# Kernel optimization log

Measured on AMD Instinct MI355X. Metric: run time of the kernel, lower is better.

## Reference

```python
import jax, jax.numpy as jnp
import numpy as np


def _flip_roll(a):
    # torch.roll(torch.flip(a, [-3,-2,-1]), (1,1,1), [-3,-2,-1])
    return jnp.roll(jnp.flip(a, axis=(-3, -2, -1)), shift=(1, 1, 1), axis=(-3, -2, -1))


def dht_3d(x):
    dims = (2, 3, 4)
    r = jnp.fft.fftn(x, axes=dims).real - jnp.fft.fftn(jnp.flip(x, axis=-1), axes=dims).imag
    norm = jnp.sqrt(jnp.sum(r * r, axis=dims, keepdims=True))
    safe = jnp.where(norm == 0, 1.0, norm)
    return jnp.where(norm != 0, r / safe, jnp.zeros_like(r))


def compl_mul3d(x1, x2):
    x1n = _flip_roll(x1)
    x2n = _flip_roll(x2)
    return 0.5 * (
        jnp.einsum('bixyz,ioxyz->boxyz', x1, x2)
        - jnp.einsum('bixyz,ioxyz->boxyz', x1n, x2n)
        + jnp.einsum('bixyz,ioxyz->boxyz', x1, x2n)
        + jnp.einsum('bixyz,ioxyz->boxyz', x1n, x2)
    )


def idht_3d(X):
    n = X.shape[2] * X.shape[3] * X.shape[4]
    return dht_3d(X) / n


def setup_inputs() -> dict:
    key = jax.random.key(0)
    k1, k2 = jax.random.split(key)
    B, Cin, Cout = 4, 32, 32
    S = 64
    M = 8
    scale = 1.0 / (Cin * Cout)
    x = jax.random.normal(k1, (B, Cin, S, S, S), dtype=jnp.float32)
    weights1 = scale * jax.random.uniform(k2, (Cin, Cout, M, M, M), dtype=jnp.float32)
    return {"x": x, "weights1": weights1}


def reference(x, weights1):
    B = x.shape[0]
    Cout = weights1.shape[1]
    m1, m2, m3 = weights1.shape[2], weights1.shape[3], weights1.shape[4]
    s1, s2, s3 = x.shape[-3], x.shape[-2], x.shape[-1]
    x_ht = dht_3d(x)
    conv = compl_mul3d(x_ht[:, :, :m1, :m2, :m3], weights1)
    out_ht = jnp.zeros((B, Cout, s1, s2, s3), dtype=x.dtype)
    out_ht = out_ht.at[:, :, :m1, :m2, :m3].set(conv)
    return idht_3d(out_ht)
```

## Files before the change

kernel.cpp:

```cpp
#include <hip/hip_runtime.h>
#include <math.h>


constexpr int NT = 262144;
constexpr float TWOPI_64 = 0.09817477042468103f;


__global__ __launch_bounds__(256) void k_fwd1(const float* __restrict__ x,
                                              float* __restrict__ S,
                                              float* __restrict__ red1p) {
  __shared__ float As[64 * 68];
  __shared__ float Bs[64 * 68];
  __shared__ float PL[32 * 65];
  __shared__ float tw1[1024];
  __shared__ float rsm[12];
  const int t = threadIdx.x;
  const int j = blockIdx.x;
  const int bc = blockIdx.y;
  const int n1a = j, n1b = (64 - j) & 63;
  const bool paired = (n1a != n1b);
  for (int u = t; u < 1024; u += 256) {
    int n3 = u >> 4, k3q = (u >> 2) & 3, jj = u & 3;
    int k3 = k3q + ((jj >> 1) << 2);
    float ang = TWOPI_64 * (float)((k3 * n3) & 63);
    tw1[u] = (jj & 1) ? sinf(ang) : cosf(ang);
  }
  const float4* xa4 = (const float4*)(x + ((size_t)bc << 18) + (n1a << 12));
  const float4* xb4 = (const float4*)(x + ((size_t)bc << 18) + (n1b << 12));
  float ssp = 0.f;
  for (int q = 0; q < 4; ++q) {
    int l4 = t + (q << 8);
    int fl = l4 << 2;
    int r = fl >> 6, c = fl & 63;
    float4 va = xa4[l4], vb = xb4[l4];
    *(float4*)&As[r * 68 + c] = va;
    *(float4*)&Bs[r * 68 + c] = vb;
    ssp += va.x * va.x + va.y * va.y + va.z * va.z + va.w * va.w;
    if (paired) ssp += vb.x * vb.x + vb.y * vb.y + vb.z * vb.z + vb.w * vb.w;
  }
  __syncthreads();
  const int n2 = t & 63;
  const int k3q = t >> 6;
  {
    float reA0 = 0, imA0 = 0, reA1 = 0, imA1 = 0;
    float reB0 = 0, imB0 = 0, reB1 = 0, imB1 = 0;
    const float4* Ar = (const float4*)&As[n2 * 68];
    const float4* Br = (const float4*)&Bs[n2 * 68];
    const float4* T4 = (const float4*)tw1;
    for (int m = 0; m < 16; ++m) {
      float4 va = Ar[m], vb = Br[m];
      float av[4] = {va.x, va.y, va.z, va.w};
      float bv[4] = {vb.x, vb.y, vb.z, vb.w};
#pragma unroll
      for (int e = 0; e < 4; ++e) {
        float4 tw = T4[(m << 4) + (e << 2) + k3q];
        float a = av[e], b = bv[e];
        reA0 += a * tw.x; imA0 -= a * tw.y;
        reB0 += b * tw.x; imB0 -= b * tw.y;
        reA1 += a * tw.z; imA1 -= a * tw.w;
        reB1 += b * tw.z; imB1 -= b * tw.w;
      }
    }
    PL[(k3q) * 65 + n2] = reA0;       PL[(8 + k3q) * 65 + n2] = imA0;
    PL[(16 + k3q) * 65 + n2] = reB0;  PL[(24 + k3q) * 65 + n2] = imB0;
    PL[(4 + k3q) * 65 + n2] = reA1;   PL[(12 + k3q) * 65 + n2] = imA1;
    PL[(20 + k3q) * 65 + n2] = reB1;  PL[(28 + k3q) * 65 + n2] = imB1;
  }
  float c1p = 0.f, c2p = 0.f;
  for (int q = 0; q < 16; ++q) {
    int l = t + (q << 8);
    int r = l >> 6, c = l & 63;
    float a = As[r * 68 + c];
    int m2 = (64 - r) & 63;
    int m3 = (64 - c) & 63;
    int m3b = (62 - c) & 63;
    c1p += a * Bs[m2 * 68 + m3];
    c2p += a * Bs[m2 * 68 + m3b];
  }
  if (paired) { c1p *= 2.f; c2p *= 2.f; }
  for (int off = 32; off; off >>= 1) {
    ssp += __shfl_down(ssp, off);
    c1p += __shfl_down(c1p, off);
    c2p += __shfl_down(c2p, off);
  }
  const int lane = t & 63, wid = t >> 6;
  if (lane == 0) { rsm[wid * 3] = ssp; rsm[wid * 3 + 1] = c1p; rsm[wid * 3 + 2] = c2p; }
  __syncthreads();
  if (t == 0) {
    red1p[((size_t)bc * 33 + j) * 3 + 0] = rsm[0] + rsm[3] + rsm[6] + rsm[9];
    red1p[((size_t)bc * 33 + j) * 3 + 1] = rsm[1] + rsm[4] + rsm[7] + rsm[10];
    red1p[((size_t)bc * 33 + j) * 3 + 2] = rsm[2] + rsm[5] + rsm[8] + rsm[11];
  }
  {
    const int k2 = t & 7;
    const int rr = t >> 3;
    const int row = rr >> 4, f = (rr >> 3) & 1, k3 = rr & 7;
    float re = 0.f, im = 0.f;
    const float* pr = &PL[rr * 65];
    const int tb = ((k2 & 3) << 2) + ((k2 >> 2) << 1);
#pragma unroll 4
    for (int n2i = 0; n2i < 64; ++n2i) {
      float v = pr[n2i];
      const float2 cs = *(const float2*)&tw1[(n2i << 4) + tb];
      re += v * cs.x; im -= v * cs.y;
    }
    const int n1row = row ? n1b : n1a;
    ((float2*)S)[(((size_t)bc * 64 + n1row) * 2 + f) * 64 + k2 * 8 + k3] =
        make_float2(re, im);
  }
}

__global__ __launch_bounds__(256) void k_fwd2s(const float* __restrict__ S,
                                               const float* __restrict__ red1p,
                                               float* __restrict__ xh) {
  __shared__ float2 U3L[256];
  __shared__ float2 tw[8 * 66];
  __shared__ float rbuf[99];
  const int t = threadIdx.x;
  const int h = blockIdx.x;
  const int bc = blockIdx.y;
  for (int u = t; u < 512; u += 256) {
    int k1 = u >> 6, n1 = u & 63;
    float ang = TWOPI_64 * (float)((k1 * n1) & 63);
    tw[k1 * 66 + n1] = make_float2(cosf(ang), sinf(ang));
  }
  if (t < 99) rbuf[t] = red1p[(size_t)bc * 99 + t];
  __syncthreads();
  {
    const int kkl = t & 15;
    const int f = (t >> 4) & 1;
    const int k1 = t >> 5;
    const int rr2 = f * 64 + h * 16 + kkl;
    const float2* Sb = (const float2*)(S + ((size_t)bc << 14));
    const float2* tk = &tw[k1 * 66];
    float re = 0.f, im = 0.f;
#pragma unroll 4
    for (int n1 = 0; n1 < 64; ++n1) {
      float2 ab = Sb[(n1 << 7) + rr2];
      float2 cs = tk[n1];
      re += ab.x * cs.x + ab.y * cs.y;
      im += ab.y * cs.x - ab.x * cs.y;
    }
    U3L[f * 128 + k1 * 16 + kkl] = make_float2(re, im);
  }
  __syncthreads();
  float ss = 0.f, c1 = 0.f, c2 = 0.f;
  for (int jj = 0; jj < 33; ++jj) {
    ss += rbuf[jj * 3];
    c1 += rbuf[jj * 3 + 1];
    c2 += rbuf[jj * 3 + 2];
  }
  float nsq = 0.5f * (float)NT * (2.f * ss + c1 - c2);
  float inv1 = nsq > 0.f ? rsqrtf(nsq) : 0.f;
  if (t < 128) {
    const int k1 = t >> 4, kkl = t & 15;
    const int kk = h * 16 + kkl;
    const int k3 = kk & 7;
    float2 U = U3L[k1 * 16 + kkl];
    float2 V = U3L[128 + k1 * 16 + kkl];
    float2 cs = tw[k3 * 66 + 1];
    float r = U.x - V.y - cs.y * (U.x + V.y) - cs.x * (U.y - V.x);
    xh[(size_t)bc * 512 + k1 * 64 + kk] = r * inv1;
  }
}

__global__ __launch_bounds__(256) void k_mixA(const float* __restrict__ xh,
                                              const float* __restrict__ w,
                                              float* __restrict__ A1,
                                              float* __restrict__ inv2q) {
  __shared__ float xsh[16384];
  __shared__ float convL[8 * 33];
  __shared__ float c64v[64], s64v[64];
  __shared__ float psum[4];
  const int t = threadIdx.x;
  const int bh = blockIdx.x;
  const int h = bh & 1;
  const int bc2 = bh >> 1;
  const int b = bc2 >> 5, o = bc2 & 31;
  if (t < 64) { float ang = TWOPI_64 * t; c64v[t] = cosf(ang); s64v[t] = sinf(ang); }
  const float4* xb4 = (const float4*)(xh + ((size_t)b << 14));
  float4* xs4 = (float4*)xsh;
  for (int q = 0; q < 16; ++q) xs4[t + (q << 8)] = xb4[t + (q << 8)];
  __syncthreads();
  const int n1m = t >> 5;
  const int col32 = t & 31;
  const int col = (h << 5) + col32;
  const int n2 = col >> 3, n3 = col & 7;
  const int k = (n1m << 6) + col;
  const int nk = (((8 - n1m) & 7) << 6) + (((8 - n2) & 7) << 3) + ((8 - n3) & 7);
  float acc = 0.f;
  const float* wb = w + ((size_t)o << 9);
#pragma unroll 4
  for (int i = 0; i < 32; ++i) {
    const float* wr = wb + ((size_t)i << 14);
    float xa = xsh[(i << 9) + k], xn = xsh[(i << 9) + nk];
    acc += (xa + xn) * wr[k] + (xa - xn) * wr[nk];
  }
  const float cval = 0.5f * acc;
  convL[n1m * 33 + col32] = cval;
  float p = cval * cval;
  for (int off = 32; off; off >>= 1) p += __shfl_down(p, off);
  if ((t & 63) == 0) psum[t >> 6] = p;
  __syncthreads();
  if (t == 0) {
    float Q = 2.f * (psum[0] + psum[1] + psum[2] + psum[3]);
    if (h == 0) { float c000 = convL[0]; Q += c000 * c000; }
    inv2q[bc2 * 2 + h] = Q;
  }
  const int q8 = t >> 5;
  float cv[8];
#pragma unroll
  for (int n1i = 0; n1i < 8; ++n1i) cv[n1i] = convL[n1i * 33 + col32];
  float2* A1p = (float2*)(A1 + ((size_t)bc2 << 13));
  for (int it = 0; it < 8; ++it) {
    const int k1 = q8 + (it << 3);
    float re = 0.f, im = 0.f;
#pragma unroll
    for (int n1i = 0; n1i < 8; ++n1i) {
      int a = (k1 * n1i) & 63;
      re += cv[n1i] * c64v[a];
      im -= cv[n1i] * s64v[a];
    }
    A1p[(k1 << 6) + col] = make_float2(re, im);
  }
}

__global__ __launch_bounds__(256) void k_expBC(const float* __restrict__ A1,
                                               const float* __restrict__ inv2q,
                                               float* __restrict__ out) {
  __shared__ float arow[128];
  __shared__ float B2[64 * 20];
  __shared__ float c64v[64], s64v[64];
  const int t = threadIdx.x;
  const int k1 = blockIdx.x;
  const int bc2 = blockIdx.y;
  const float q0 = inv2q[bc2 * 2], q1 = inv2q[bc2 * 2 + 1];
  if (t < 64) { float ang = TWOPI_64 * t; c64v[t] = cosf(ang); s64v[t] = sinf(ang); }
  if (t < 128) arow[t] = A1[((size_t)bc2 << 13) + (k1 << 7) + t];
  __syncthreads();
  {
    const int k2 = t & 63;
    const int g = t >> 6;
    const int f = g & 1;
    const int n3h = (g >> 1) << 2;
    float acc[4] = {0, 0, 0, 0};
    for (int n2i = 0; n2i < 8; ++n2i) {
      int a_ = (k2 * n2i) & 63;
      float tc = c64v[a_], ts = s64v[a_];
      const float4* ar4 = (const float4*)&arow[((n2i << 3) + n3h) << 1];
      float4 p0 = ar4[0];
      float4 p1 = ar4[1];
      if (f == 0) {
        acc[0] += p0.x * tc + p0.y * ts;
        acc[1] += p0.z * tc + p0.w * ts;
        acc[2] += p1.x * tc + p1.y * ts;
        acc[3] += p1.z * tc + p1.w * ts;
      } else {
        acc[0] += p0.y * tc - p0.x * ts;
        acc[1] += p0.w * tc - p0.z * ts;
        acc[2] += p1.y * tc - p1.x * ts;
        acc[3] += p1.w * tc - p1.z * ts;
      }
    }
    *(float4*)&B2[k2 * 20 + (f << 3) + n3h] = make_float4(acc[0], acc[1], acc[2], acc[3]);
  }
  __syncthreads();
  {
    const int k3 = t & 63;
    const int wid = t >> 6;
    float C1r[8], C2r[8];
#pragma unroll
    for (int n3 = 0; n3 < 8; ++n3) {
      int a0 = (k3 * n3) & 63;
      int a1 = (k3 * (n3 + 1)) & 63;
      C1r[n3] = c64v[a0] - s64v[a1];
      C2r[n3] = s64v[a0] - c64v[a1];
    }
    float nsq = 0.5f * (float)NT * (q0 + q1);
    const float sc = nsq > 0.f ? 1.f / (sqrtf(nsq) * (float)NT) : 0.f;
    float* dst = out + ((size_t)bc2 << 18) + (k1 << 12);
    for (int it = 0; it < 16; ++it) {
      int k2 = (wid << 4) + it;
      const float4* br4 = (const float4*)&B2[k2 * 20];
      float4 r0 = br4[0], r1 = br4[1], r2 = br4[2], r3 = br4[3];
      float acc = r0.x * C1r[0] + r0.y * C1r[1] + r0.z * C1r[2] + r0.w * C1r[3]
                + r1.x * C1r[4] + r1.y * C1r[5] + r1.z * C1r[6] + r1.w * C1r[7]
                + r2.x * C2r[0] + r2.y * C2r[1] + r2.z * C2r[2] + r2.w * C2r[3]
                + r3.x * C2r[4] + r3.y * C2r[5] + r3.z * C2r[6] + r3.w * C2r[7];
      dst[(k2 << 6) + k3] = acc * sc;
    }
  }
}

extern "C" void kernel_launch(void* const* d_in, const int* in_sizes, int n_in,
                              void* d_out, int out_size, void* d_ws, size_t ws_size,
                              hipStream_t stream) {
  const float* x = (const float*)d_in[0];
  const float* w = (const float*)d_in[1];
  float* out = (float*)d_out;
  float* ws = (float*)d_ws;
  float* S     = ws;
  float* red1p = ws + 2097152;
  float* xh    = ws + 2109824;
  float* inv2q = ws + 2175360;
  float* A1    = ws + 2175616;

  k_fwd1 <<<dim3(33, 128), 256, 0, stream>>>(x, S, red1p);
  k_fwd2s<<<dim3(4, 128),  256, 0, stream>>>(S, red1p, xh);
  k_mixA <<<dim3(256),     256, 0, stream>>>(xh, w, A1, inv2q);
  k_expBC<<<dim3(64, 128), 256, 0, stream>>>(A1, inv2q, out);
}
```

Baseline: 271.3 us.

## Fuse four stage kernels into one persistent kernel with grid barriers

Replaces the four separate launches with a single persistent kernel of 528 blocks that loops over the former grid work and separates the stages with atomic-counter grid barriers. It also swaps the per-element twiddle table lookups in the second forward DFT for a complex-rotation recurrence, and changes the PL padding so it can be read as float4. The mix stage now reads xh straight from global memory instead of staging it in shared memory. This removes launch gaps and tail effects between stages, but it depends on all 528 blocks being co-resident, pays for spin-wait barriers, and the recurrence may build up rounding error.

```diff
diff --git a/kernel.cpp b/kernel.cpp
--- a/kernel.cpp
+++ b/kernel.cpp
@@ -4,290 +4,317 @@
 
 constexpr int NT = 262144;
 constexpr float TWOPI_64 = 0.09817477042468103f;
-
-
-__global__ __launch_bounds__(256) void k_fwd1(const float* __restrict__ x,
-                                              float* __restrict__ S,
-                                              float* __restrict__ red1p) {
-  __shared__ float As[64 * 68];
-  __shared__ float Bs[64 * 68];
-  __shared__ float PL[32 * 65];
-  __shared__ float tw1[1024];
-  __shared__ float rsm[12];
+constexpr int NBLK = 528;
+
+
+__global__ void k_zero(int* __restrict__ cnt) {
+  if (threadIdx.x < 8) cnt[threadIdx.x] = 0;
+}
+
+__device__ __forceinline__ void gridbar(int* cnt, int ph) {
+  __syncthreads();
+  if (threadIdx.x == 0) {
+    __threadfence();
+    atomicAdd(&cnt[ph], 1);
+    while (atomicAdd(&cnt[ph], 0) < NBLK) __builtin_amdgcn_s_sleep(4);
+    __threadfence();
+  }
+  __syncthreads();
+}
+
+__global__ __launch_bounds__(256, 3) void k_mega(
+    const float* __restrict__ x, const float* __restrict__ w,
+    float* __restrict__ out, float* __restrict__ S, float* __restrict__ red1p,
+    float* __restrict__ xh, float* __restrict__ inv2q, float* __restrict__ A1,
+    int* __restrict__ cnt) {
+  __shared__ float smem[11916];
   const int t = threadIdx.x;
-  const int j = blockIdx.x;
-  const int bc = blockIdx.y;
-  const int n1a = j, n1b = (64 - j) & 63;
-  const bool paired = (n1a != n1b);
-  for (int u = t; u < 1024; u += 256) {
-    int n3 = u >> 4, k3q = (u >> 2) & 3, jj = u & 3;
-    int k3 = k3q + ((jj >> 1) << 2);
-    float ang = TWOPI_64 * (float)((k3 * n3) & 63);
-    tw1[u] = (jj & 1) ? sinf(ang) : cosf(ang);
-  }
-  const float4* xa4 = (const float4*)(x + ((size_t)bc << 18) + (n1a << 12));
-  const float4* xb4 = (const float4*)(x + ((size_t)bc << 18) + (n1b << 12));
-  float ssp = 0.f;
-  for (int q = 0; q < 4; ++q) {
-    int l4 = t + (q << 8);
-    int fl = l4 << 2;
-    int r = fl >> 6, c = fl & 63;
-    float4 va = xa4[l4], vb = xb4[l4];
-    *(float4*)&As[r * 68 + c] = va;
-    *(float4*)&Bs[r * 68 + c] = vb;
-    ssp += va.x * va.x + va.y * va.y + va.z * va.z + va.w * va.w;
-    if (paired) ssp += vb.x * vb.x + vb.y * vb.y + vb.z * vb.z + vb.w * vb.w;
-  }
-  __syncthreads();
-  const int n2 = t & 63;
-  const int k3q = t >> 6;
+  const int blk = blockIdx.x;
+
   {
-    float reA0 = 0, imA0 = 0, reA1 = 0, imA1 = 0;
-    float reB0 = 0, imB0 = 0, reB1 = 0, imB1 = 0;
-    const float4* Ar = (const float4*)&As[n2 * 68];
-    const float4* Br = (const float4*)&Bs[n2 * 68];
-    const float4* T4 = (const float4*)tw1;
-    for (int m = 0; m < 16; ++m) {
-      float4 va = Ar[m], vb = Br[m];
-      float av[4] = {va.x, va.y, va.z, va.w};
-      float bv[4] = {vb.x, vb.y, vb.z, vb.w};
+    float* As  = smem;
+    float* Bs  = smem + 4352;
+    float* PL  = smem + 8704;
+    float* tw1 = smem + 10880;
+    float* rsm = smem + 11904;
+    for (int u = t; u < 1024; u += 256) {
+      int n3 = u >> 4, k3q = (u >> 2) & 3, jj = u & 3;
+      int k3 = k3q + ((jj >> 1) << 2);
+      float ang = TWOPI_64 * (float)((k3 * n3) & 63);
+      tw1[u] = (jj & 1) ? sinf(ang) : cosf(ang);
+    }
+    const int k2s = t & 7;
+    const float angs = TWOPI_64 * (float)k2s;
+    const float dc2 = cosf(angs), ds2 = sinf(angs);
+    const int n2 = t & 63;
+    const int k3q = t >> 6;
+
+    for (int vb = blk; vb < 4224; vb += NBLK) {
+      const int bc = vb / 33;
+      const int j = vb - bc * 33;
+      const int n1a = j, n1b = (64 - j) & 63;
+      const bool paired = (n1a != n1b);
+      const float4* xa4 = (const float4*)(x + ((size_t)bc << 18) + (n1a << 12));
+      const float4* xb4 = (const float4*)(x + ((size_t)bc << 18) + (n1b << 12));
+      float ssp = 0.f;
+      for (int q = 0; q < 4; ++q) {
+        int l4 = t + (q << 8);
+        int fl = l4 << 2;
+        int r = fl >> 6, c = fl & 63;
+        float4 va = xa4[l4], vb4 = xb4[l4];
+        *(float4*)&As[r * 68 + c] = va;
+        *(float4*)&Bs[r * 68 + c] = vb4;
+        ssp += va.x * va.x + va.y * va.y + va.z * va.z + va.w * va.w;
+        if (paired) ssp += vb4.x * vb4.x + vb4.y * vb4.y + vb4.z * vb4.z + vb4.w * vb4.w;
+      }
+      __syncthreads();
+      {
+        float reA0 = 0, imA0 = 0, reA1 = 0, imA1 = 0;
+        float reB0 = 0, imB0 = 0, reB1 = 0, imB1 = 0;
+        const float4* Ar = (const float4*)&As[n2 * 68];
+        const float4* Br = (const float4*)&Bs[n2 * 68];
+        const float4* T4 = (const float4*)tw1;
+        for (int m = 0; m < 16; ++m) {
+          float4 va = Ar[m], vb4 = Br[m];
+          float av[4] = {va.x, va.y, va.z, va.w};
+          float bv[4] = {vb4.x, vb4.y, vb4.z, vb4.w};
 #pragma unroll
-      for (int e = 0; e < 4; ++e) {
-        float4 tw = T4[(m << 4) + (e << 2) + k3q];
-        float a = av[e], b = bv[e];
-        reA0 += a * tw.x; imA0 -= a * tw.y;
-        reB0 += b * tw.x; imB0 -= b * tw.y;
-        reA1 += a * tw.z; imA1 -= a * tw.w;
-        reB1 += b * tw.z; imB1 -= b * tw.w;
-      }
-    }
-    PL[(k3q) * 65 + n2] = reA0;       PL[(8 + k3q) * 65 + n2] = imA0;
-    PL[(16 + k3q) * 65 + n2] = reB0;  PL[(24 + k3q) * 65 + n2] = imB0;
-    PL[(4 + k3q) * 65 + n2] = reA1;   PL[(12 + k3q) * 65 + n2] = imA1;
-    PL[(20 + k3q) * 65 + n2] = reB1;  PL[(28 + k3q) * 65 + n2] = imB1;
-  }
-  float c1p = 0.f, c2p = 0.f;
-  for (int q = 0; q < 16; ++q) {
-    int l = t + (q << 8);
-    int r = l >> 6, c = l & 63;
-    float a = As[r * 68 + c];
-    int m2 = (64 - r) & 63;
-    int m3 = (64 - c) & 63;
-    int m3b = (62 - c) & 63;
-    c1p += a * Bs[m2 * 68 + m3];
-    c2p += a * Bs[m2 * 68 + m3b];
-  }
-  if (paired) { c1p *= 2.f; c2p *= 2.f; }
-  for (int off = 32; off; off >>= 1) {
-    ssp += __shfl_down(ssp, off);
-    c1p += __shfl_down(c1p, off);
-    c2p += __shfl_down(c2p, off);
-  }
-  const int lane = t & 63, wid = t >> 6;
-  if (lane == 0) { rsm[wid * 3] = ssp; rsm[wid * 3 + 1] = c1p; rsm[wid * 3 + 2] = c2p; }
-  __syncthreads();
-  if (t == 0) {
-    red1p[((size_t)bc * 33 + j) * 3 + 0] = rsm[0] + rsm[3] + rsm[6] + rsm[9];
-    red1p[((size_t)bc * 33 + j) * 3 + 1] = rsm[1] + rsm[4] + rsm[7] + rsm[10];
-    red1p[((size_t)bc * 33 + j) * 3 + 2] = rsm[2] + rsm[5] + rsm[8] + rsm[11];
-  }
+          for (int e = 0; e < 4; ++e) {
+            float4 tw = T4[(m << 4) + (e << 2) + k3q];
+            float a = av[e], b = bv[e];
+            reA0 += a * tw.x; imA0 -= a * tw.y;
+            reB0 += b * tw.x; imB0 -= b * tw.y;
+            reA1 += a * tw.z; imA1 -= a * tw.w;
+            reB1 += b * tw.z; imB1 -= b * tw.w;
+          }
+        }
+        PL[(k3q) * 68 + n2] = reA0;       PL[(8 + k3q) * 68 + n2] = imA0;
+        PL[(16 + k3q) * 68 + n2] = reB0;  PL[(24 + k3q) * 68 + n2] = imB0;
+        PL[(4 + k3q) * 68 + n2] = reA1;   PL[(12 + k3q) * 68 + n2] = imA1;
+        PL[(20 + k3q) * 68 + n2] = reB1;  PL[(28 + k3q) * 68 + n2] = imB1;
+      }
+      float c1p = 0.f, c2p = 0.f;
+      for (int q = 0; q < 16; ++q) {
+        int l = t + (q << 8);
+        int r = l >> 6, c = l & 63;
+        float a = As[r * 68 + c];
+        int m2 = (64 - r) & 63;
+        int m3 = (64 - c) & 63;
+        int m3b = (62 - c) & 63;
+        c1p += a * Bs[m2 * 68 + m3];
+        c2p += a * Bs[m2 * 68 + m3b];
+      }
+      if (paired) { c1p *= 2.f; c2p *= 2.f; }
+      for (int off = 32; off; off >>= 1) {
+        ssp += __shfl_down(ssp, off);
+        c1p += __shfl_down(c1p, off);
+        c2p += __shfl_down(c2p, off);
+      }
+      const int lane = t & 63, wid = t >> 6;
+      if (lane == 0) { rsm[wid * 3] = ssp; rsm[wid * 3 + 1] = c1p; rsm[wid * 3 + 2] = c2p; }
+      __syncthreads();
+      if (t == 0) {
+        red1p[((size_t)bc * 33 + j) * 3 + 0] = rsm[0] + rsm[3] + rsm[6] + rsm[9];
+        red1p[((size_t)bc * 33 + j) * 3 + 1] = rsm[1] + rsm[4] + rsm[7] + rsm[10];
+        red1p[((size_t)bc * 33 + j) * 3 + 2] = rsm[2] + rsm[5] + rsm[8] + rsm[11];
+      }
+      {
+        const int rr = t >> 3;
+        const int row = rr >> 4, f = (rr >> 3) & 1, k3 = rr & 7;
+        float rc = 1.f, rs = 0.f, re = 0.f, im = 0.f;
+        const float4* pr4 = (const float4*)&PL[rr * 68];
+#pragma unroll 4
+        for (int m = 0; m < 16; ++m) {
+          float4 v = pr4[m];
+          re += v.x * rc; im -= v.x * rs;
+          { float nc = rc * dc2 - rs * ds2; rs = rs * dc2 + rc * ds2; rc = nc; }
+          re += v.y * rc; im -= v.y * rs;
+          { float nc = rc * dc2 - rs * ds2; rs = rs * dc2 + rc * ds2; rc = nc; }
+          re += v.z * rc; im -= v.z * rs;
+          { float nc = rc * dc2 - rs * ds2; rs = rs * dc2 + rc * ds2; rc = nc; }
+          re += v.w * rc; im -= v.w * rs;
+          { float nc = rc * dc2 - rs * ds2; rs = rs * dc2 + rc * ds2; rc = nc; }
+        }
+        const int n1row = row ? n1b : n1a;
+        ((float2*)S)[(((size_t)bc * 64 + n1row) * 2 + f) * 64 + k2s * 8 + k3] =
+            make_float2(re, im);
+      }
+    }
+  }
+  gridbar(cnt, 0);
+
+  if (blk < 512) {
+    const int h = blk & 3;
+    const int bc = blk >> 2;
+    float2* U3L = (float2*)smem;
+    float2* tw2 = (float2*)(smem + 512);
+    float* rbuf = smem + 1568;
+    for (int u = t; u < 512; u += 256) {
+      int k1 = u >> 6, n1 = u & 63;
+      float ang = TWOPI_64 * (float)((k1 * n1) & 63);
+      tw2[k1 * 66 + n1] = make_float2(cosf(ang), sinf(ang));
+    }
+    if (t < 99) rbuf[t] = red1p[(size_t)bc * 99 + t];
+    __syncthreads();
+    {
+      const int kkl = t & 15;
+      const int f = (t >> 4) & 1;
+      const int k1 = t >> 5;
+      const int rr2 = f * 64 + h * 16 + kkl;
+      const float2* Sb = (const float2*)(S + ((size_t)bc << 14));
+      const float2* tk = &tw2[k1 * 66];
+      float re = 0.f, im = 0.f;
+#pragma unroll 4
+      for (int n1 = 0; n1 < 64; ++n1) {
+        float2 ab = Sb[(n1 << 7) + rr2];
+        float2 cs = tk[n1];
+        re += ab.x * cs.x + ab.y * cs.y;
+        im += ab.y * cs.x - ab.x * cs.y;
+      }
+      U3L[f * 128 + k1 * 16 + kkl] = make_float2(re, im);
+    }
+    __syncthreads();
+    float ss = 0.f, c1 = 0.f, c2 = 0.f;
+    for (int jj = 0; jj < 33; ++jj) {
+      ss += rbuf[jj * 3];
+      c1 += rbuf[jj * 3 + 1];
+      c2 += rbuf[jj * 3 + 2];
+    }
+    float nsq = 0.5f * (float)NT * (2.f * ss + c1 - c2);
+    float inv1 = nsq > 0.f ? rsqrtf(nsq) : 0.f;
+    if (t < 128) {
+      const int k1w = t >> 4, kkl2 = t & 15;
+      const int kk = h * 16 + kkl2;
+      const int k3 = kk & 7;
+      float2 U = U3L[k1w * 16 + kkl2];
+      float2 V = U3L[128 + k1w * 16 + kkl2];
+      float2 cs = tw2[k3 * 66 + 1];
+      float r = U.x - V.y - cs.y * (U.x + V.y) - cs.x * (U.y - V.x);
+      xh[(size_t)bc * 512 + k1w * 64 + kk] = r * inv1;
+    }
+  }
+  gridbar(cnt, 1);
+
+  if (((blk & 1) == 0) && blk < 512) {
+    const int bh = blk >> 1;
+    const int h = bh & 1;
+    const int bc2 = bh >> 1;
+    const int b = bc2 >> 5, o = bc2 & 31;
+    float* convL = smem;
+    float* c64v = smem + 264;
+    float* s64v = smem + 328;
+    float* psum = smem + 392;
+    if (t < 64) { float ang = TWOPI_64 * t; c64v[t] = cosf(ang); s64v[t] = sinf(ang); }
+    const float* xg = xh + ((size_t)b << 14);
+    const int n1m = t >> 5;
+    const int col32 = t & 31;
+    const int col = (h << 5) + col32;
+    const int n2 = col >> 3, n3 = col & 7;
+    const int k = (n1m << 6) + col;
+    const int nk = (((8 - n1m) & 7) << 6) + (((8 - n2) & 7) << 3) + ((8 - n3) & 7);
+    float acc = 0.f;
+    const float* wb = w + ((size_t)o << 9);
+#pragma unroll 4
+    for (int i = 0; i < 32; ++i) {
+      const float* wr = wb + ((size_t)i << 14);
+      float xa = xg[(i << 9) + k], xn = xg[(i << 9) + nk];
+      acc += (xa + xn) * wr[k] + (xa - xn) * wr[nk];
+    }
+    const float cval = 0.5f * acc;
+    convL[n1m * 33 + col32] = cval;
+    float p = cval * cval;
+    for (int off = 32; off; off >>= 1) p += __shfl_down(p, off);
+    if ((t & 63) == 0) psum[t >> 6] = p;
+    __syncthreads();
+    if (t == 0) {
+      float Q = 2.f * (psum[0] + psum[1] + psum[2] + psum[3]);
+      if (h == 0) { float c000 = convL[0]; Q += c000 * c000; }
+      inv2q[bc2 * 2 + h] = Q;
+    }
+    const int q8 = t >> 5;
+    float cv[8];
+#pragma unroll
+    for (int n1i = 0; n1i < 8; ++n1i) cv[n1i] = convL[n1i * 33 + col32];
+    float2* A1p = (float2*)(A1 + ((size_t)bc2 << 13));
+    for (int it = 0; it < 8; ++it) {
+      const int k1 = q8 + (it << 3);
+      float re = 0.f, im = 0.f;
+#pragma unroll
+      for (int n1i = 0; n1i < 8; ++n1i) {
+        int a = (k1 * n1i) & 63;
+        re += cv[n1i] * c64v[a];
+        im -= cv[n1i] * s64v[a];
+      }
+      A1p[(k1 << 6) + col] = make_float2(re, im);
+    }
+  }
+  gridbar(cnt, 2);
+
   {
-    const int k2 = t & 7;
-    const int rr = t >> 3;
-    const int row = rr >> 4, f = (rr >> 3) & 1, k3 = rr & 7;
-    float re = 0.f, im = 0.f;
-    const float* pr = &PL[rr * 65];
-    const int tb = ((k2 & 3) << 2) + ((k2 >> 2) << 1);
-#pragma unroll 4
-    for (int n2i = 0; n2i < 64; ++n2i) {
-      float v = pr[n2i];
-      const float2 cs = *(const float2*)&tw1[(n2i << 4) + tb];
-      re += v * cs.x; im -= v * cs.y;
-    }
-    const int n1row = row ? n1b : n1a;
-    ((float2*)S)[(((size_t)bc * 64 + n1row) * 2 + f) * 64 + k2 * 8 + k3] =
-        make_float2(re, im);
-  }
-}
-
-__global__ __launch_bounds__(256) void k_fwd2s(const float* __restrict__ S,
-                                               const float* __restrict__ red1p,
-                                               float* __restrict__ xh) {
-  __shared__ float2 U3L[256];
-  __shared__ float2 tw[8 * 66];
-  __shared__ float rbuf[99];
-  const int t = threadIdx.x;
-  const int h = blockIdx.x;
-  const int bc = blockIdx.y;
-  for (int u = t; u < 512; u += 256) {
-    int k1 = u >> 6, n1 = u & 63;
-    float ang = TWOPI_64 * (float)((k1 * n1) & 63);
-    tw[k1 * 66 + n1] = make_float2(cosf(ang), sinf(ang));
-  }
-  if (t < 99) rbuf[t] = red1p[(size_t)bc * 99 + t];
-  __syncthreads();
-  {
-    const int kkl = t & 15;
-    const int f = (t >> 4) & 1;
-    const int k1 = t >> 5;
-    const int rr2 = f * 64 + h * 16 + kkl;
-    const float2* Sb = (const float2*)(S + ((size_t)bc << 14));
-    const float2* tk = &tw[k1 * 66];
-    float re = 0.f, im = 0.f;
-#pragma unroll 4
-    for (int n1 = 0; n1 < 64; ++n1) {
-      float2 ab = Sb[(n1 << 7) + rr2];
-      float2 cs = tk[n1];
-      re += ab.x * cs.x + ab.y * cs.y;
-      im += ab.y * cs.x - ab.x * cs.y;
-    }
-    U3L[f * 128 + k1 * 16 + kkl] = make_float2(re, im);
-  }
-  __syncthreads();
-  float ss = 0.f, c1 = 0.f, c2 = 0.f;
-  for (int jj = 0; jj < 33; ++jj) {
-    ss += rbuf[jj * 3];
-    c1 += rbuf[jj * 3 + 1];
-    c2 += rbuf[jj * 3 + 2];
-  }
-  float nsq = 0.5f * (float)NT * (2.f * ss + c1 - c2);
-  float inv1 = nsq > 0.f ? rsqrtf(nsq) : 0.f;
-  if (t < 128) {
-    const int k1 = t >> 4, kkl = t & 15;
-    const int kk = h * 16 + kkl;
-    const int k3 = kk & 7;
-    float2 U = U3L[k1 * 16 + kkl];
-    float2 V = U3L[128 + k1 * 16 + kkl];
-    float2 cs = tw[k3 * 66 + 1];
-    float r = U.x - V.y - cs.y * (U.x + V.y) - cs.x * (U.y - V.x);
-    xh[(size_t)bc * 512 + k1 * 64 + kk] = r * inv1;
-  }
-}
-
-__global__ __launch_bounds__(256) void k_mixA(const float* __restrict__ xh,
-                                              const float* __restrict__ w,
-                                              float* __restrict__ A1,
-                                              float* __restrict__ inv2q) {
-  __shared__ float xsh[16384];
-  __shared__ float convL[8 * 33];
-  __shared__ float c64v[64], s64v[64];
-  __shared__ float psum[4];
-  const int t = threadIdx.x;
-  const int bh = blockIdx.x;
-  const int h = bh & 1;
-  const int bc2 = bh >> 1;
-  const int b = bc2 >> 5, o = bc2 & 31;
-  if (t < 64) { float ang = TWOPI_64 * t; c64v[t] = cosf(ang); s64v[t] = sinf(ang); }
-  const float4* xb4 = (const float4*)(xh + ((size_t)b << 14));
-  float4* xs4 = (float4*)xsh;
-  for (int q = 0; q < 16; ++q) xs4[t + (q << 8)] = xb4[t + (q << 8)];
-  __syncthreads();
-  const int n1m = t >> 5;
-  const int col32 = t & 31;
-  const int col = (h << 5) + col32;
-  const int n2 = col >> 3, n3 = col & 7;
-  const int k = (n1m << 6) + col;
-  const int nk = (((8 - n1m) & 7) << 6) + (((8 - n2) & 7) << 3) + ((8 - n3) & 7);
-  float acc = 0.f;
-  const float* wb = w + ((size_t)o << 9);
-#pragma unroll 4
-  for (int i = 0; i < 32; ++i) {
-    const float* wr = wb + ((size_t)i << 14);
-    float xa = xsh[(i << 9) + k], xn = xsh[(i << 9) + nk];
-    acc += (xa + xn) * wr[k] + (xa - xn) * wr[nk];
-  }
-  const float cval = 0.5f * acc;
-  convL[n1m * 33 + col32] = cval;
-  float p = cval * cval;
-  for (int off = 32; off; off >>= 1) p += __shfl_down(p, off);
-  if ((t & 63) == 0) psum[t >> 6] = p;
-  __syncthreads();
-  if (t == 0) {
-    float Q = 2.f * (psum[0] + psum[1] + psum[2] + psum[3]);
-    if (h == 0) { float c000 = convL[0]; Q += c000 * c000; }
-    inv2q[bc2 * 2 + h] = Q;
-  }
-  const int q8 = t >> 5;
-  float cv[8];
-#pragma unroll
-  for (int n1i = 0; n1i < 8; ++n1i) cv[n1i] = convL[n1i * 33 + col32];
-  float2* A1p = (float2*)(A1 + ((size_t)bc2 << 13));
-  for (int it = 0; it < 8; ++it) {
-    const int k1 = q8 + (it << 3);
-    float re = 0.f, im = 0.f;
-#pragma unroll
-    for (int n1i = 0; n1i < 8; ++n1i) {
-      int a = (k1 * n1i) & 63;
-      re += cv[n1i] * c64v[a];
-      im -= cv[n1i] * s64v[a];
-    }
-    A1p[(k1 << 6) + col] = make_float2(re, im);
-  }
-}
-
-__global__ __launch_bounds__(256) void k_expBC(const float* __restrict__ A1,
-                                               const float* __restrict__ inv2q,
-                                               float* __restrict__ out) {
-  __shared__ float arow[128];
-  __shared__ float B2[64 * 20];
-  __shared__ float c64v[64], s64v[64];
-  const int t = threadIdx.x;
-  const int k1 = blockIdx.x;
-  const int bc2 = blockIdx.y;
-  const float q0 = inv2q[bc2 * 2], q1 = inv2q[bc2 * 2 + 1];
-  if (t < 64) { float ang = TWOPI_64 * t; c64v[t] = cosf(ang); s64v[t] = sinf(ang); }
-  if (t < 128) arow[t] = A1[((size_t)bc2 << 13) + (k1 << 7) + t];
-  __syncthreads();
-  {
-    const int k2 = t & 63;
-    const int g = t >> 6;
-    const int f = g & 1;
-    const int n3h = (g >> 1) << 2;
-    float acc[4] = {0, 0, 0, 0};
-    for (int n2i = 0; n2i < 8; ++n2i) {
-      int a_ = (k2 * n2i) & 63;
-      float tc = c64v[a_], ts = s64v[a_];
-      const float4* ar4 = (const float4*)&arow[((n2i << 3) + n3h) << 1];
-      float4 p0 = ar4[0];
-      float4 p1 = ar4[1];
-      if (f == 0) {
-        acc[0] += p0.x * tc + p0.y * ts;
-        acc[1] += p0.z * tc + p0.w * ts;
-        acc[2] += p1.x * tc + p1.y * ts;
-        acc[3] += p1.z * tc + p1.w * ts;
-      } else {
-        acc[0] += p0.y * tc - p0.x * ts;
-        acc[1] += p0.w * tc - p0.z * ts;
-        acc[2] += p1.y * tc - p1.x * ts;
-        acc[3] += p1.w * tc - p1.z * ts;
-      }
-    }
-    *(float4*)&B2[k2 * 20 + (f << 3) + n3h] = make_float4(acc[0], acc[1], acc[2], acc[3]);
-  }
-  __syncthreads();
-  {
-    const int k3 = t & 63;
-    const int wid = t >> 6;
+    float* arow = smem;
+    float* B2 = smem + 128;
+    float* c64v = smem + 1408;
+    float* s64v = smem + 1472;
+    if (t < 64) { float ang = TWOPI_64 * t; c64v[t] = cosf(ang); s64v[t] = sinf(ang); }
+    __syncthreads();
+    const int k3c = t & 63;
+    const int widc = t >> 6;
     float C1r[8], C2r[8];
 #pragma unroll
     for (int n3 = 0; n3 < 8; ++n3) {
-      int a0 = (k3 * n3) & 63;
-      int a1 = (k3 * (n3 + 1)) & 63;
+      int a0 = (k3c * n3) & 63;
+      int a1 = (k3c * (n3 + 1)) & 63;
       C1r[n3] = c64v[a0] - s64v[a1];
       C2r[n3] = s64v[a0] - c64v[a1];
     }
-    float nsq = 0.5f * (float)NT * (q0 + q1);
-    const float sc = nsq > 0.f ? 1.f / (sqrtf(nsq) * (float)NT) : 0.f;
-    float* dst = out + ((size_t)bc2 << 18) + (k1 << 12);
-    for (int it = 0; it < 16; ++it) {
-      int k2 = (wid << 4) + it;
-      const float4* br4 = (const float4*)&B2[k2 * 20];
-      float4 r0 = br4[0], r1 = br4[1], r2 = br4[2], r3 = br4[3];
-      float acc = r0.x * C1r[0] + r0.y * C1r[1] + r0.z * C1r[2] + r0.w * C1r[3]
-                + r1.x * C1r[4] + r1.y * C1r[5] + r1.z * C1r[6] + r1.w * C1r[7]
-                + r2.x * C2r[0] + r2.y * C2r[1] + r2.z * C2r[2] + r2.w * C2r[3]
-                + r3.x * C2r[4] + r3.y * C2r[5] + r3.z * C2r[6] + r3.w * C2r[7];
-      dst[(k2 << 6) + k3] = acc * sc;
+    for (int vb = blk; vb < 8192; vb += NBLK) {
+      const int k1 = vb & 63, bc2 = vb >> 6;
+      if (t < 128) arow[t] = A1[((size_t)bc2 << 13) + (k1 << 7) + t];
+      __syncthreads();
+      {
+        const int k2 = t & 63;
+        const int g = t >> 6;
+        const int f = g & 1;
+        const int n3h = (g >> 1) << 2;
+        float accv[4] = {0, 0, 0, 0};
+        for (int n2i = 0; n2i < 8; ++n2i) {
+          int a_ = (k2 * n2i) & 63;
+          float tc = c64v[a_], ts = s64v[a_];
+          const float4* ar4 = (const float4*)&arow[((n2i << 3) + n3h) << 1];
+          float4 p0 = ar4[0];
+          float4 p1 = ar4[1];
+          if (f == 0) {
+            accv[0] += p0.x * tc + p0.y * ts;
+            accv[1] += p0.z * tc + p0.w * ts;
+            accv[2] += p1.x * tc + p1.y * ts;
+            accv[3] += p1.z * tc + p1.w * ts;
+          } else {
+            accv[0] += p0.y * tc - p0.x * ts;
+            accv[1] += p0.w * tc - p0.z * ts;
+            accv[2] += p1.y * tc - p1.x * ts;
+            accv[3] += p1.w * tc - p1.z * ts;
+          }
+        }
+        *(float4*)&B2[k2 * 20 + (f << 3) + n3h] =
+            make_float4(accv[0], accv[1], accv[2], accv[3]);
+      }
+      __syncthreads();
+      {
+        float q0 = inv2q[bc2 * 2], q1 = inv2q[bc2 * 2 + 1];
+        float nsq = 0.5f * (float)NT * (q0 + q1);
+        const float sc = nsq > 0.f ? 1.f / (sqrtf(nsq) * (float)NT) : 0.f;
+        float* dst = out + ((size_t)bc2 << 18) + (k1 << 12);
+        for (int it = 0; it < 16; ++it) {
+          int k2 = (widc << 4) + it;
+          const float4* br4 = (const float4*)&B2[k2 * 20];
+          float4 r0 = br4[0], r1 = br4[1], r2 = br4[2], r3 = br4[3];
+          float acc = r0.x * C1r[0] + r0.y * C1r[1] + r0.z * C1r[2] + r0.w * C1r[3]
+                    + r1.x * C1r[4] + r1.y * C1r[5] + r1.z * C1r[6] + r1.w * C1r[7]
+                    + r2.x * C2r[0] + r2.y * C2r[1] + r2.z * C2r[2] + r2.w * C2r[3]
+                    + r3.x * C2r[4] + r3.y * C2r[5] + r3.z * C2r[6] + r3.w * C2r[7];
+          dst[(k2 << 6) + k3c] = acc * sc;
+        }
+      }
     }
   }
 }
@@ -304,9 +331,8 @@
   float* xh    = ws + 2109824;
   float* inv2q = ws + 2175360;
   float* A1    = ws + 2175616;
-
-  k_fwd1 <<<dim3(33, 128), 256, 0, stream>>>(x, S, red1p);
-  k_fwd2s<<<dim3(4, 128),  256, 0, stream>>>(S, red1p, xh);
-  k_mixA <<<dim3(256),     256, 0, stream>>>(xh, w, A1, inv2q);
-  k_expBC<<<dim3(64, 128), 256, 0, stream>>>(A1, inv2q, out);
+  int*   cnt   = (int*)(ws + 3224192);
+
+  k_zero<<<1, 64, 0, stream>>>(cnt);
+  k_mega<<<dim3(NBLK), dim3(256), 0, stream>>>(x, w, out, S, red1p, xh, inv2q, A1, cnt);
 }
```

After: 438.7 us. 1.62x slower.

## Fuse spectral mix with inverse transform; use twiddle recurrence in forward pass

Applied to the files above, without the earlier changes.

The channel-mixing kernel and the inverse-expansion kernel are merged into one kernel launched on a (2,128) grid. Each block recomputes the full 512-point mode mix for its (batch, out-channel), computes the normalisation locally, and writes 32 k1 planes of the output. This drops the A1/inv2q workspace round trip, one launch, and the earlier xh shared-memory staging. In k_fwd1 the final 64-point DFT now generates twiddles with a complex rotation recurrence over float4 loads instead of reading them from the shared-memory table, and the PL row pitch is padded to 68. In exchange, the large output write now comes from only 256 blocks of 4 waves each, which may underuse memory bandwidth. The recurrence also adds a small amount of rounding drift.

```diff
diff --git a/kernel.cpp b/kernel.cpp
--- a/kernel.cpp
+++ b/kernel.cpp
@@ -11,7 +11,7 @@
                                               float* __restrict__ red1p) {
   __shared__ float As[64 * 68];
   __shared__ float Bs[64 * 68];
-  __shared__ float PL[32 * 65];
+  __shared__ float PL[32 * 68];
   __shared__ float tw1[1024];
   __shared__ float rsm[12];
   const int t = threadIdx.x;
@@ -25,6 +25,9 @@
     float ang = TWOPI_64 * (float)((k3 * n3) & 63);
     tw1[u] = (jj & 1) ? sinf(ang) : cosf(ang);
   }
+  const int k2s = t & 7;
+  const float angs = TWOPI_64 * (float)k2s;
+  const float dc2 = cosf(angs), ds2 = sinf(angs);
   const float4* xa4 = (const float4*)(x + ((size_t)bc << 18) + (n1a << 12));
   const float4* xb4 = (const float4*)(x + ((size_t)bc << 18) + (n1b << 12));
   float ssp = 0.f;
@@ -61,10 +64,10 @@
         reB1 += b * tw.z; imB1 -= b * tw.w;
       }
     }
-    PL[(k3q) * 65 + n2] = reA0;       PL[(8 + k3q) * 65 + n2] = imA0;
-    PL[(16 + k3q) * 65 + n2] = reB0;  PL[(24 + k3q) * 65 + n2] = imB0;
-    PL[(4 + k3q) * 65 + n2] = reA1;   PL[(12 + k3q) * 65 + n2] = imA1;
-    PL[(20 + k3q) * 65 + n2] = reB1;  PL[(28 + k3q) * 65 + n2] = imB1;
+    PL[(k3q) * 68 + n2] = reA0;       PL[(8 + k3q) * 68 + n2] = imA0;
+    PL[(16 + k3q) * 68 + n2] = reB0;  PL[(24 + k3q) * 68 + n2] = imB0;
+    PL[(4 + k3q) * 68 + n2] = reA1;   PL[(12 + k3q) * 68 + n2] = imA1;
+    PL[(20 + k3q) * 68 + n2] = reB1;  PL[(28 + k3q) * 68 + n2] = imB1;
   }
   float c1p = 0.f, c2p = 0.f;
   for (int q = 0; q < 16; ++q) {
@@ -92,20 +95,24 @@
     red1p[((size_t)bc * 33 + j) * 3 + 2] = rsm[2] + rsm[5] + rsm[8] + rsm[11];
   }
   {
-    const int k2 = t & 7;
     const int rr = t >> 3;
     const int row = rr >> 4, f = (rr >> 3) & 1, k3 = rr & 7;
-    float re = 0.f, im = 0.f;
-    const float* pr = &PL[rr * 65];
-    const int tb = ((k2 & 3) << 2) + ((k2 >> 2) << 1);
+    float rc = 1.f, rs = 0.f, re = 0.f, im = 0.f;
+    const float4* pr4 = (const float4*)&PL[rr * 68];
 #pragma unroll 4
-    for (int n2i = 0; n2i < 64; ++n2i) {
-      float v = pr[n2i];
-      const float2 cs = *(const float2*)&tw1[(n2i << 4) + tb];
-      re += v * cs.x; im -= v * cs.y;
+    for (int m = 0; m < 16; ++m) {
+      float4 v = pr4[m];
+      re += v.x * rc; im -= v.x * rs;
+      { float nc = rc * dc2 - rs * ds2; rs = rs * dc2 + rc * ds2; rc = nc; }
+      re += v.y * rc; im -= v.y * rs;
+      { float nc = rc * dc2 - rs * ds2; rs = rs * dc2 + rc * ds2; rc = nc; }
+      re += v.z * rc; im -= v.z * rs;
+      { float nc = rc * dc2 - rs * ds2; rs = rs * dc2 + rc * ds2; rc = nc; }
+      re += v.w * rc; im -= v.w * rs;
+      { float nc = rc * dc2 - rs * ds2; rs = rs * dc2 + rc * ds2; rc = nc; }
     }
     const int n1row = row ? n1b : n1a;
-    ((float2*)S)[(((size_t)bc * 64 + n1row) * 2 + f) * 64 + k2 * 8 + k3] =
+    ((float2*)S)[(((size_t)bc * 64 + n1row) * 2 + f) * 64 + k2s * 8 + k3] =
         make_float2(re, im);
   }
 }
@@ -164,130 +171,121 @@
   }
 }
 
-__global__ __launch_bounds__(256) void k_mixA(const float* __restrict__ xh,
-                                              const float* __restrict__ w,
-                                              float* __restrict__ A1,
-                                              float* __restrict__ inv2q) {
-  __shared__ float xsh[16384];
-  __shared__ float convL[8 * 33];
+__global__ __launch_bounds__(256) void k_mixexp(const float* __restrict__ xh,
+                                                const float* __restrict__ w,
+                                                float* __restrict__ out) {
+  __shared__ float convL[8 * 66];
+  __shared__ float A1L[32 * 132];
+  __shared__ float B2w[4 * 64 * 20];
   __shared__ float c64v[64], s64v[64];
   __shared__ float psum[4];
   const int t = threadIdx.x;
-  const int bh = blockIdx.x;
-  const int h = bh & 1;
-  const int bc2 = bh >> 1;
+  const int h = blockIdx.x;
+  const int bc2 = blockIdx.y;
   const int b = bc2 >> 5, o = bc2 & 31;
   if (t < 64) { float ang = TWOPI_64 * t; c64v[t] = cosf(ang); s64v[t] = sinf(ang); }
-  const float4* xb4 = (const float4*)(xh + ((size_t)b << 14));
-  float4* xs4 = (float4*)xsh;
-  for (int q = 0; q < 16; ++q) xs4[t + (q << 8)] = xb4[t + (q << 8)];
-  __syncthreads();
-  const int n1m = t >> 5;
-  const int col32 = t & 31;
-  const int col = (h << 5) + col32;
-  const int n2 = col >> 3, n3 = col & 7;
-  const int k = (n1m << 6) + col;
-  const int nk = (((8 - n1m) & 7) << 6) + (((8 - n2) & 7) << 3) + ((8 - n3) & 7);
-  float acc = 0.f;
+  const float* xg = xh + ((size_t)b << 14);
+  const int col = t & 63;
+  const int n1m = t >> 6;
+  const int n2c = col >> 3, n3c = col & 7;
+  const int nkc = (((8 - n2c) & 7) << 3) + ((8 - n3c) & 7);
+  const int k0 = t;
+  const int nk0 = (((8 - n1m) & 7) << 6) + nkc;
+  const int k1p = t + 256;
+  const int nk1 = (((8 - (n1m + 4)) & 7) << 6) + nkc;
+  float acc0 = 0.f, acc1 = 0.f;
   const float* wb = w + ((size_t)o << 9);
 #pragma unroll 4
   for (int i = 0; i < 32; ++i) {
     const float* wr = wb + ((size_t)i << 14);
-    float xa = xsh[(i << 9) + k], xn = xsh[(i << 9) + nk];
-    acc += (xa + xn) * wr[k] + (xa - xn) * wr[nk];
-  }
-  const float cval = 0.5f * acc;
-  convL[n1m * 33 + col32] = cval;
-  float p = cval * cval;
+    const float* xi = xg + (i << 9);
+    float xa0 = xi[k0], xn0 = xi[nk0];
+    float xa1 = xi[k1p], xn1 = xi[nk1];
+    acc0 += (xa0 + xn0) * wr[k0] + (xa0 - xn0) * wr[nk0];
+    acc1 += (xa1 + xn1) * wr[k1p] + (xa1 - xn1) * wr[nk1];
+  }
+  const float c0 = 0.5f * acc0, c1v = 0.5f * acc1;
+  convL[n1m * 66 + col] = c0;
+  convL[(n1m + 4) * 66 + col] = c1v;
+  float p = c0 * c0 + c1v * c1v;
   for (int off = 32; off; off >>= 1) p += __shfl_down(p, off);
   if ((t & 63) == 0) psum[t >> 6] = p;
   __syncthreads();
-  if (t == 0) {
-    float Q = 2.f * (psum[0] + psum[1] + psum[2] + psum[3]);
-    if (h == 0) { float c000 = convL[0]; Q += c000 * c000; }
-    inv2q[bc2 * 2 + h] = Q;
-  }
-  const int q8 = t >> 5;
+  const float S2 = psum[0] + psum[1] + psum[2] + psum[3];
+  const float c000 = convL[0];
+  const float nsq = 0.5f * (float)NT * (2.f * S2 + c000 * c000);
+  const float sc = nsq > 0.f ? 1.f / (sqrtf(nsq) * (float)NT) : 0.f;
+  const int wid = t >> 6, l = t & 63;
   float cv[8];
 #pragma unroll
-  for (int n1i = 0; n1i < 8; ++n1i) cv[n1i] = convL[n1i * 33 + col32];
-  float2* A1p = (float2*)(A1 + ((size_t)bc2 << 13));
+  for (int n1 = 0; n1 < 8; ++n1) cv[n1] = convL[n1 * 66 + l];
+#pragma unroll
   for (int it = 0; it < 8; ++it) {
-    const int k1 = q8 + (it << 3);
+    const int k1l = wid * 8 + it;
+    const int k1g = (h << 5) + k1l;
     float re = 0.f, im = 0.f;
 #pragma unroll
-    for (int n1i = 0; n1i < 8; ++n1i) {
-      int a = (k1 * n1i) & 63;
-      re += cv[n1i] * c64v[a];
-      im -= cv[n1i] * s64v[a];
-    }
-    A1p[(k1 << 6) + col] = make_float2(re, im);
-  }
-}
-
-__global__ __launch_bounds__(256) void k_expBC(const float* __restrict__ A1,
-                                               const float* __restrict__ inv2q,
-                                               float* __restrict__ out) {
-  __shared__ float arow[128];
-  __shared__ float B2[64 * 20];
-  __shared__ float c64v[64], s64v[64];
-  const int t = threadIdx.x;
-  const int k1 = blockIdx.x;
-  const int bc2 = blockIdx.y;
-  const float q0 = inv2q[bc2 * 2], q1 = inv2q[bc2 * 2 + 1];
-  if (t < 64) { float ang = TWOPI_64 * t; c64v[t] = cosf(ang); s64v[t] = sinf(ang); }
-  if (t < 128) arow[t] = A1[((size_t)bc2 << 13) + (k1 << 7) + t];
-  __syncthreads();
-  {
-    const int k2 = t & 63;
-    const int g = t >> 6;
-    const int f = g & 1;
-    const int n3h = (g >> 1) << 2;
-    float acc[4] = {0, 0, 0, 0};
+    for (int n1 = 0; n1 < 8; ++n1) {
+      int a = (k1g * n1) & 63;
+      re += cv[n1] * c64v[a];
+      im -= cv[n1] * s64v[a];
+    }
+    A1L[k1l * 132 + 2 * l] = re;
+    A1L[k1l * 132 + 2 * l + 1] = im;
+  }
+  asm volatile("s_waitcnt lgkmcnt(0)" ::: "memory");
+  float csc[8], css[8];
+#pragma unroll
+  for (int n2i = 0; n2i < 8; ++n2i) {
+    int a = (l * n2i) & 63;
+    csc[n2i] = c64v[a]; css[n2i] = s64v[a];
+  }
+  float C1r[8], C2r[8];
+#pragma unroll
+  for (int n3 = 0; n3 < 8; ++n3) {
+    int a0 = (l * n3) & 63;
+    int a1 = (l * (n3 + 1)) & 63;
+    C1r[n3] = c64v[a0] - s64v[a1];
+    C2r[n3] = s64v[a0] - c64v[a1];
+  }
+  float* B2r = &B2w[wid * 1280];
+  float* outb = out + ((size_t)bc2 << 18);
+  for (int it = 0; it < 8; ++it) {
+    const int k1l = wid * 8 + it;
+    const int k1g = (h << 5) + k1l;
+    const float* Arow = &A1L[k1l * 132];
+    float f0[8] = {0, 0, 0, 0, 0, 0, 0, 0};
+    float f1[8] = {0, 0, 0, 0, 0, 0, 0, 0};
+#pragma unroll
     for (int n2i = 0; n2i < 8; ++n2i) {
-      int a_ = (k2 * n2i) & 63;
-      float tc = c64v[a_], ts = s64v[a_];
-      const float4* ar4 = (const float4*)&arow[((n2i << 3) + n3h) << 1];
-      float4 p0 = ar4[0];
-      float4 p1 = ar4[1];
-      if (f == 0) {
-        acc[0] += p0.x * tc + p0.y * ts;
-        acc[1] += p0.z * tc + p0.w * ts;
-        acc[2] += p1.x * tc + p1.y * ts;
-        acc[3] += p1.z * tc + p1.w * ts;
-      } else {
-        acc[0] += p0.y * tc - p0.x * ts;
-        acc[1] += p0.w * tc - p0.z * ts;
-        acc[2] += p1.y * tc - p1.x * ts;
-        acc[3] += p1.w * tc - p1.z * ts;
-      }
-    }
-    *(float4*)&B2[k2 * 20 + (f << 3) + n3h] = make_float4(acc[0], acc[1], acc[2], acc[3]);
-  }
-  __syncthreads();
-  {
-    const int k3 = t & 63;
-    const int wid = t >> 6;
-    float C1r[8], C2r[8];
-#pragma unroll
-    for (int n3 = 0; n3 < 8; ++n3) {
-      int a0 = (k3 * n3) & 63;
-      int a1 = (k3 * (n3 + 1)) & 63;
-      C1r[n3] = c64v[a0] - s64v[a1];
-      C2r[n3] = s64v[a0] - c64v[a1];
-    }
-    float nsq = 0.5f * (float)NT * (q0 + q1);
-    const float sc = nsq > 0.f ? 1.f / (sqrtf(nsq) * (float)NT) : 0.f;
-    float* dst = out + ((size_t)bc2 << 18) + (k1 << 12);
-    for (int it = 0; it < 16; ++it) {
-      int k2 = (wid << 4) + it;
-      const float4* br4 = (const float4*)&B2[k2 * 20];
-      float4 r0 = br4[0], r1 = br4[1], r2 = br4[2], r3 = br4[3];
+      const float4* a4 = (const float4*)&Arow[n2i << 4];
+      float4 q0 = a4[0], q1 = a4[1], q2 = a4[2], q3 = a4[3];
+      float tc = csc[n2i], ts = css[n2i];
+      f0[0] += q0.x * tc + q0.y * ts;  f1[0] += q0.y * tc - q0.x * ts;
+      f0[1] += q0.z * tc + q0.w * ts;  f1[1] += q0.w * tc - q0.z * ts;
+      f0[2] += q1.x * tc + q1.y * ts;  f1[2] += q1.y * tc - q1.x * ts;
+      f0[3] += q1.z * tc + q1.w * ts;  f1[3] += q1.w * tc - q1.z * ts;
+      f0[4] += q2.x * tc + q2.y * ts;  f1[4] += q2.y * tc - q2.x * ts;
+      f0[5] += q2.z * tc + q2.w * ts;  f1[5] += q2.w * tc - q2.z * ts;
+      f0[6] += q3.x * tc + q3.y * ts;  f1[6] += q3.y * tc - q3.x * ts;
+      f0[7] += q3.z * tc + q3.w * ts;  f1[7] += q3.w * tc - q3.z * ts;
+    }
+    float* br = &B2r[l * 20];
+    *(float4*)&br[0]  = make_float4(f0[0], f0[1], f0[2], f0[3]);
+    *(float4*)&br[4]  = make_float4(f0[4], f0[5], f0[6], f0[7]);
+    *(float4*)&br[8]  = make_float4(f1[0], f1[1], f1[2], f1[3]);
+    *(float4*)&br[12] = make_float4(f1[4], f1[5], f1[6], f1[7]);
+    asm volatile("s_waitcnt lgkmcnt(0)" ::: "memory");
+    float* dst = outb + ((size_t)k1g << 12);
+#pragma unroll 4
+    for (int k2 = 0; k2 < 64; ++k2) {
+      const float4* b4 = (const float4*)&B2r[k2 * 20];
+      float4 r0 = b4[0], r1 = b4[1], r2 = b4[2], r3 = b4[3];
       float acc = r0.x * C1r[0] + r0.y * C1r[1] + r0.z * C1r[2] + r0.w * C1r[3]
                 + r1.x * C1r[4] + r1.y * C1r[5] + r1.z * C1r[6] + r1.w * C1r[7]
                 + r2.x * C2r[0] + r2.y * C2r[1] + r2.z * C2r[2] + r2.w * C2r[3]
                 + r3.x * C2r[4] + r3.y * C2r[5] + r3.z * C2r[6] + r3.w * C2r[7];
-      dst[(k2 << 6) + k3] = acc * sc;
+      dst[(k2 << 6) + l] = acc * sc;
     }
   }
 }
@@ -302,11 +300,8 @@
   float* S     = ws;
   float* red1p = ws + 2097152;
   float* xh    = ws + 2109824;
-  float* inv2q = ws + 2175360;
-  float* A1    = ws + 2175616;
-
-  k_fwd1 <<<dim3(33, 128), 256, 0, stream>>>(x, S, red1p);
-  k_fwd2s<<<dim3(4, 128),  256, 0, stream>>>(S, red1p, xh);
-  k_mixA <<<dim3(256),     256, 0, stream>>>(xh, w, A1, inv2q);
-  k_expBC<<<dim3(64, 128), 256, 0, stream>>>(A1, inv2q, out);
+
+  k_fwd1  <<<dim3(33, 128), 256, 0, stream>>>(x, S, red1p);
+  k_fwd2s <<<dim3(4, 128),  256, 0, stream>>>(S, red1p, xh);
+  k_mixexp<<<dim3(2, 128),  256, 0, stream>>>(xh, w, out);
 }
```

Result: slower. 298.7 us (+10.1%).
